# Performance work log

Measured on AMD Instinct MI355X. Metric: run time of the kernel, lower is better.

The kernel has to match this reference:

```python
import jax, jax.numpy as jnp
import numpy as np

NUM_SITES = 64
PHYS_DIM = 2
BOND_DIM = 32
BATCH = 65536


def _build_mps(num_sites, phys_dim, bond_dim, seed=0):
    """Replicates ImprovedMPS._initialize_tensors + _canonical_form, then
    zero-pads ragged cores into a dense [S, D, p, D] stack."""
    rng = np.random.default_rng(seed)
    tensors = []
    cur = 1
    for i in range(num_sites):
        if i == 0:
            nb = min(bond_dim, phys_dim)
            shape = (1, phys_dim, nb)
            cur = nb
        elif i == num_sites - 1:
            shape = (cur, phys_dim, 1)
        else:
            nb = min(bond_dim, cur * phys_dim)
            shape = (cur, phys_dim, nb)
            cur = nb
        ld, rd = shape[0] * shape[1], shape[2]
        m = (rng.standard_normal((ld, rd)) * 0.1).astype(np.float32)
        if ld >= rd:
            q, _ = np.linalg.qr(m)
            t = q.reshape(shape)
        else:
            q, _ = np.linalg.qr(m.T)
            t = q.T.reshape(shape)
        tensors.append(t.astype(np.float32))
    # left-canonical sweep
    for i in range(num_sites - 1):
        l, p, r = tensors[i].shape
        q, rr = np.linalg.qr(tensors[i].reshape(l * p, r))
        tensors[i] = q.reshape(l, p, q.shape[1]).astype(np.float32)
        nl, npd, nr = tensors[i + 1].shape
        tensors[i + 1] = (rr @ tensors[i + 1].reshape(nl, npd * nr)).reshape(rr.shape[0], npd, nr).astype(np.float32)
    # zero-pad ragged bonds into dense stack [S, D, p, D]
    A = np.zeros((num_sites, bond_dim, phys_dim, bond_dim), dtype=np.float32)
    for i, t in enumerate(tensors):
        l, p, r = t.shape
        A[i, :l, :, :r] = t
    return A


def setup_inputs() -> dict:
    key = jax.random.key(0)
    x_batch = jax.random.normal(key, (BATCH, NUM_SITES, PHYS_DIM), dtype=jnp.float32)
    A = jnp.asarray(_build_mps(NUM_SITES, PHYS_DIM, BOND_DIM))
    return {"x_batch": x_batch, "A": A}


def reference(x_batch, A):
    # x_batch: [B, S, p]; A: [S, D, p, D] (zero-padded ragged MPS cores)
    B = x_batch.shape[0]
    D = A.shape[1]
    # left_vector starts as ones(B,1) in the ragged view == one-hot e0 in padded view
    left0 = jnp.zeros((B, D), dtype=x_batch.dtype).at[:, 0].set(1.0)
    xs = jnp.moveaxis(x_batch, 1, 0)  # [S, B, p]

    def step(left, inp):
        A_i, x_i = inp  # [D, p, D], [B, p]
        # fuses: contracted = einsum('bp,lpd->bld'); left = einsum('bl,bld->bd')
        left = jnp.einsum('bl,bp,lpd->bd', left, x_i, A_i)
        return left, None

    left, _ = jax.lax.scan(step, left0, (A, xs))
    return left[:, :1]  # last core has right bond 1 -> only col 0 is nonzero
```

## Files before the change

### kernel.cpp

```cpp
#include <hip/hip_runtime.h>


typedef _Float16 half8 __attribute__((ext_vector_type(8)));
typedef _Float16 half4 __attribute__((ext_vector_type(4)));
typedef float floatx16 __attribute__((ext_vector_type(16)));
typedef float f32x4 __attribute__((ext_vector_type(4)));

#define NPAIRS 32
#define GCH 8192
#define XSTRIDE 129

__global__ void mps_prep_pair(const float* __restrict__ A, _Float16* __restrict__ Gf) {
    __shared__ float sA0[2048], sA1[2048], sG[4096];
    const int P = blockIdx.x, tid = threadIdx.x;
    const float* a0p = A + (size_t)(2 * P) * 2048;
    const float* a1p = A + (size_t)(2 * P + 1) * 2048;
#pragma unroll
    for (int i = 0; i < 8; ++i) {
        sA0[tid + 256 * i] = a0p[tid + 256 * i];
        sA1[tid + 256 * i] = a1p[tid + 256 * i];
    }
    __syncthreads();
    {
        const int l = tid >> 3, pq = (tid >> 1) & 3, dh16 = (tid & 1) * 16;
        const int p = pq >> 1, q = pq & 1;
        float accv[16];
#pragma unroll
        for (int dd = 0; dd < 16; ++dd) accv[dd] = 0.f;
        for (int m = 0; m < 32; ++m) {
            const float av = sA0[l * 64 + p * 32 + m];
            const float* bp = &sA1[m * 64 + q * 32 + dh16];
#pragma unroll
            for (int dd = 0; dd < 16; ++dd) accv[dd] += av * bp[dd];
        }
#pragma unroll
        for (int dd = 0; dd < 16; ++dd) sG[l * 128 + pq * 32 + dh16 + dd] = accv[dd];
    }
    __syncthreads();
    const int lane = tid & 63;
    const int h    = lane >> 5;
    const int d    = lane & 31;
#pragma unroll
    for (int pass = 0; pass < 2; ++pass) {
        const int kf = (tid >> 6) + pass * 4;
        const int pq = kf >> 1, lh = kf & 1;
        half8 v;
#pragma unroll
        for (int e = 0; e < 8; ++e) {
            const int l = 16 * lh + (e & 3) + 8 * (e >> 2) + 4 * h;
            v[e] = (_Float16)sG[l * 128 + pq * 32 + d];
        }
        reinterpret_cast<half8*>(Gf)[((size_t)P * 8 + kf) * 64 + lane] = v;
    }
}

#define MF32(A_, B_, C_) __builtin_amdgcn_mfma_f32_32x32x16_f16(A_, B_, C_, 0, 0, 0)

#define STAGEG(C, BUF)                                                        \
    {                                                                         \
        _Pragma("unroll")                                                     \
        for (int r_ = 0; r_ < 4; ++r_) {                                      \
            const int rec_ = r_ * 4 + wid;                                    \
            const _Float16* g_ = Gf + (size_t)(C) * GCH + rec_ * 512 + lane * 8; \
            __builtin_amdgcn_global_load_lds(                                 \
                (const __attribute__((address_space(1))) void*)g_,            \
                (__attribute__((address_space(3))) void*)&smG[(BUF) * GCH + rec_ * 512], \
                16, 0, 0);                                                    \
        }                                                                     \
    }

#define PAIRDO(BUF, LP, P)                                                    \
    {                                                                         \
        const half4 xq_ = smX[(P) * XSTRIDE + r];                             \
        const _Float16 w00_ = xq_[0] * xq_[2];                                \
        const _Float16 w01_ = xq_[0] * xq_[3];                                \
        const _Float16 w10_ = xq_[1] * xq_[2];                                \
        const _Float16 w11_ = xq_[1] * xq_[3];                                \
        half8 G_[8];                                                          \
        _Pragma("unroll")                                                     \
        for (int f_ = 0; f_ < 8; ++f_)                                        \
            G_[f_] = *(const half8*)&smG[(BUF) * GCH + (((LP) * 8 + f_) * 64 + lane) * 8]; \
        half8 FA0_, FA1_;                                                     \
        _Pragma("unroll")                                                     \
        for (int i_ = 0; i_ < 8; ++i_) {                                      \
            FA0_[i_] = (_Float16)acc[i_];                                     \
            FA1_[i_] = (_Float16)acc[8 + i_];                                 \
        }                                                                     \
        floatx16 t_;                                                          \
        t_ = MF32(G_[0], FA0_ * w00_, zv);                                    \
        t_ = MF32(G_[1], FA1_ * w00_, t_);                                    \
        t_ = MF32(G_[2], FA0_ * w01_, t_);                                    \
        t_ = MF32(G_[3], FA1_ * w01_, t_);                                    \
        t_ = MF32(G_[4], FA0_ * w10_, t_);                                    \
        t_ = MF32(G_[5], FA1_ * w10_, t_);                                    \
        t_ = MF32(G_[6], FA0_ * w11_, t_);                                    \
        t_ = MF32(G_[7], FA1_ * w11_, t_);                                    \
        acc = t_;                                                             \
    }

#define CHUNK(C, BUF)                                                         \
    {                                                                         \
        if ((C) < 15) STAGEG((C) + 1, 1 - (BUF));                             \
        PAIRDO(BUF, 0, 2 * (C))                                               \
        PAIRDO(BUF, 1, 2 * (C) + 1)                                           \
        __syncthreads();                                                      \
    }

__global__ __launch_bounds__(256, 2) void mps_main(const float* __restrict__ x,
                                                   const _Float16* __restrict__ Gf,
                                                   float* __restrict__ out) {
    __shared__ __align__(16) _Float16 smG[2 * GCH];
    __shared__ __align__(8)  half4    smX[32 * XSTRIDE];

    const int tid  = threadIdx.x;
    const int lane = tid & 63;
    const int wid  = tid >> 6;
    const int brow = blockIdx.x * 128;
    const int col  = lane & 31;
    const int r    = wid * 32 + col;

    STAGEG(0, 0);

#pragma unroll
    for (int i = 0; i < 16; ++i) {
        const int j   = i * 256 + tid;
        const int row = j >> 5, q = j & 31;
        const f32x4 v = *(const f32x4*)(x + (size_t)(brow + row) * 128 + 4 * q);
        half4 hv;
        hv[0] = (_Float16)v[0]; hv[1] = (_Float16)v[1];
        hv[2] = (_Float16)v[2]; hv[3] = (_Float16)v[3];
        smX[q * XSTRIDE + row] = hv;
    }

    floatx16 zv;
#pragma unroll
    for (int i = 0; i < 16; ++i) zv[i] = 0.f;

    floatx16 acc;
#pragma unroll
    for (int i = 0; i < 16; ++i) acc[i] = 0.f;
    if (lane < 32) acc[0] = 1.f;

    __syncthreads();

    CHUNK(0, 0)   CHUNK(1, 1)   CHUNK(2, 0)   CHUNK(3, 1)
    CHUNK(4, 0)   CHUNK(5, 1)   CHUNK(6, 0)   CHUNK(7, 1)
    CHUNK(8, 0)   CHUNK(9, 1)   CHUNK(10, 0)  CHUNK(11, 1)
    CHUNK(12, 0)  CHUNK(13, 1)  CHUNK(14, 0)  CHUNK(15, 1)

    if (lane < 32) out[brow + wid * 32 + lane] = acc[0];
}

extern "C" void kernel_launch(void* const* d_in, const int* in_sizes, int n_in,
                              void* d_out, int out_size, void* d_ws, size_t ws_size,
                              hipStream_t stream) {
    const float* x = (const float*)d_in[0];
    const float* A = (const float*)d_in[1];
    float* outp = (float*)d_out;
    _Float16* Gf = (_Float16*)d_ws;

    hipLaunchKernelGGL(mps_prep_pair, dim3(NPAIRS), dim3(256), 0, stream, A, Gf);
    hipLaunchKernelGGL(mps_main, dim3(65536 / 128), dim3(256), 0, stream, x, Gf, outp);
}
```

Baseline: 28.77 us.

## Split pair-core staging between LDS and direct register prefetch from global

The main kernel now stages only half of each fused pair-core (the p=0 fragments) into LDS. The other half comes straight from global memory into registers, prefetched one pair ahead with ping-pong register arrays. Because each LDS chunk now covers four pairs instead of two, the number of barriers and LDS traffic are halved. The cost is more VGPR pressure and per-lane global loads on the MFMA critical path. The prep kernel also moves to 512 threads, each doing half the output columns.

```diff
diff --git a/kernel.cpp b/kernel.cpp
--- a/kernel.cpp
+++ b/kernel.cpp
@@ -7,7 +7,7 @@
 typedef float f32x4 __attribute__((ext_vector_type(4)));
 
 #define NPAIRS 32
-#define GCH 8192
+#define GCHH 8192
 #define XSTRIDE 129
 
 __global__ void mps_prep_pair(const float* __restrict__ A, _Float16* __restrict__ Gf) {
@@ -16,42 +16,41 @@
     const float* a0p = A + (size_t)(2 * P) * 2048;
     const float* a1p = A + (size_t)(2 * P + 1) * 2048;
 #pragma unroll
-    for (int i = 0; i < 8; ++i) {
-        sA0[tid + 256 * i] = a0p[tid + 256 * i];
-        sA1[tid + 256 * i] = a1p[tid + 256 * i];
+    for (int i = 0; i < 4; ++i) {
+        sA0[tid + 512 * i] = a0p[tid + 512 * i];
+        sA1[tid + 512 * i] = a1p[tid + 512 * i];
     }
     __syncthreads();
     {
-        const int l = tid >> 3, pq = (tid >> 1) & 3, dh16 = (tid & 1) * 16;
+        const int item = tid >> 1;
+        const int l = item >> 3, pq = (item >> 1) & 3, dh16 = (item & 1) * 16;
+        const int ddb = (tid & 1) * 8;
         const int p = pq >> 1, q = pq & 1;
-        float accv[16];
+        float accv[8];
 #pragma unroll
-        for (int dd = 0; dd < 16; ++dd) accv[dd] = 0.f;
+        for (int dd = 0; dd < 8; ++dd) accv[dd] = 0.f;
         for (int m = 0; m < 32; ++m) {
             const float av = sA0[l * 64 + p * 32 + m];
-            const float* bp = &sA1[m * 64 + q * 32 + dh16];
+            const float* bp = &sA1[m * 64 + q * 32 + dh16 + ddb];
 #pragma unroll
-            for (int dd = 0; dd < 16; ++dd) accv[dd] += av * bp[dd];
+            for (int dd = 0; dd < 8; ++dd) accv[dd] += av * bp[dd];
         }
 #pragma unroll
-        for (int dd = 0; dd < 16; ++dd) sG[l * 128 + pq * 32 + dh16 + dd] = accv[dd];
+        for (int dd = 0; dd < 8; ++dd) sG[l * 128 + pq * 32 + dh16 + ddb + dd] = accv[dd];
     }
     __syncthreads();
     const int lane = tid & 63;
     const int h    = lane >> 5;
     const int d    = lane & 31;
+    const int kf   = tid >> 6;
+    const int pq   = kf >> 1, lh = kf & 1;
+    half8 v;
 #pragma unroll
-    for (int pass = 0; pass < 2; ++pass) {
-        const int kf = (tid >> 6) + pass * 4;
-        const int pq = kf >> 1, lh = kf & 1;
-        half8 v;
-#pragma unroll
-        for (int e = 0; e < 8; ++e) {
-            const int l = 16 * lh + (e & 3) + 8 * (e >> 2) + 4 * h;
-            v[e] = (_Float16)sG[l * 128 + pq * 32 + d];
-        }
-        reinterpret_cast<half8*>(Gf)[((size_t)P * 8 + kf) * 64 + lane] = v;
+    for (int e = 0; e < 8; ++e) {
+        const int l = 16 * lh + (e & 3) + 8 * (e >> 2) + 4 * h;
+        v[e] = (_Float16)sG[l * 128 + pq * 32 + d];
     }
+    reinterpret_cast<half8*>(Gf)[((size_t)P * 8 + kf) * 64 + lane] = v;
 }
 
 #define MF32(A_, B_, C_) __builtin_amdgcn_mfma_f32_32x32x16_f16(A_, B_, C_, 0, 0, 0)
@@ -61,25 +60,29 @@
         _Pragma("unroll")                                                     \
         for (int r_ = 0; r_ < 4; ++r_) {                                      \
             const int rec_ = r_ * 4 + wid;                                    \
-            const _Float16* g_ = Gf + (size_t)(C) * GCH + rec_ * 512 + lane * 8; \
+            const int pl_ = rec_ >> 2, kf_ = rec_ & 3;                        \
+            const _Float16* g_ = Gf + ((((size_t)(C) * 4 + pl_) * 8 + kf_) * 64 + lane) * 8; \
             __builtin_amdgcn_global_load_lds(                                 \
                 (const __attribute__((address_space(1))) void*)g_,            \
-                (__attribute__((address_space(3))) void*)&smG[(BUF) * GCH + rec_ * 512], \
+                (__attribute__((address_space(3))) void*)&smG[(BUF) * GCHH + rec_ * 512], \
                 16, 0, 0);                                                    \
         }                                                                     \
     }
 
-#define PAIRDO(BUF, LP, P)                                                    \
+#define PAIRDO(BUF, LP, P, GP, GN)                                            \
     {                                                                         \
         const half4 xq_ = smX[(P) * XSTRIDE + r];                             \
         const _Float16 w00_ = xq_[0] * xq_[2];                                \
         const _Float16 w01_ = xq_[0] * xq_[3];                                \
         const _Float16 w10_ = xq_[1] * xq_[2];                                \
         const _Float16 w11_ = xq_[1] * xq_[3];                                \
-        half8 G_[8];                                                          \
+        half8 GL_[4];                                                         \
         _Pragma("unroll")                                                     \
-        for (int f_ = 0; f_ < 8; ++f_)                                        \
-            G_[f_] = *(const half8*)&smG[(BUF) * GCH + (((LP) * 8 + f_) * 64 + lane) * 8]; \
+        for (int f_ = 0; f_ < 4; ++f_)                                        \
+            GL_[f_] = *(const half8*)&smG[(BUF) * GCHH + (((LP) * 4 + f_) * 64 + lane) * 8]; \
+        _Pragma("unroll")                                                     \
+        for (int f_ = 0; f_ < 4; ++f_)                                        \
+            GN[f_] = gfp[((((P) + 1) & 31) * 8 + 4 + f_) * 64 + lane];        \
         half8 FA0_, FA1_;                                                     \
         _Pragma("unroll")                                                     \
         for (int i_ = 0; i_ < 8; ++i_) {                                      \
@@ -87,29 +90,31 @@
             FA1_[i_] = (_Float16)acc[8 + i_];                                 \
         }                                                                     \
         floatx16 t_;                                                          \
-        t_ = MF32(G_[0], FA0_ * w00_, zv);                                    \
-        t_ = MF32(G_[1], FA1_ * w00_, t_);                                    \
-        t_ = MF32(G_[2], FA0_ * w01_, t_);                                    \
-        t_ = MF32(G_[3], FA1_ * w01_, t_);                                    \
-        t_ = MF32(G_[4], FA0_ * w10_, t_);                                    \
-        t_ = MF32(G_[5], FA1_ * w10_, t_);                                    \
-        t_ = MF32(G_[6], FA0_ * w11_, t_);                                    \
-        t_ = MF32(G_[7], FA1_ * w11_, t_);                                    \
+        t_ = MF32(GL_[0], FA0_ * w00_, zv);                                   \
+        t_ = MF32(GL_[1], FA1_ * w00_, t_);                                   \
+        t_ = MF32(GL_[2], FA0_ * w01_, t_);                                   \
+        t_ = MF32(GL_[3], FA1_ * w01_, t_);                                   \
+        t_ = MF32(GP[0], FA0_ * w10_, t_);                                    \
+        t_ = MF32(GP[1], FA1_ * w10_, t_);                                    \
+        t_ = MF32(GP[2], FA0_ * w11_, t_);                                    \
+        t_ = MF32(GP[3], FA1_ * w11_, t_);                                    \
         acc = t_;                                                             \
     }
 
 #define CHUNK(C, BUF)                                                         \
     {                                                                         \
-        if ((C) < 15) STAGEG((C) + 1, 1 - (BUF));                             \
-        PAIRDO(BUF, 0, 2 * (C))                                               \
-        PAIRDO(BUF, 1, 2 * (C) + 1)                                           \
+        if ((C) < 7) STAGEG((C) + 1, 1 - (BUF));                              \
+        PAIRDO(BUF, 0, 4 * (C) + 0, Ga, Gb)                                   \
+        PAIRDO(BUF, 1, 4 * (C) + 1, Gb, Ga)                                   \
+        PAIRDO(BUF, 2, 4 * (C) + 2, Ga, Gb)                                   \
+        PAIRDO(BUF, 3, 4 * (C) + 3, Gb, Ga)                                   \
         __syncthreads();                                                      \
     }
 
 __global__ __launch_bounds__(256, 2) void mps_main(const float* __restrict__ x,
                                                    const _Float16* __restrict__ Gf,
                                                    float* __restrict__ out) {
-    __shared__ __align__(16) _Float16 smG[2 * GCH];
+    __shared__ __align__(16) _Float16 smG[2 * GCHH];
     __shared__ __align__(8)  half4    smX[32 * XSTRIDE];
 
     const int tid  = threadIdx.x;
@@ -118,6 +123,8 @@
     const int brow = blockIdx.x * 128;
     const int col  = lane & 31;
     const int r    = wid * 32 + col;
+
+    const half8* gfp = reinterpret_cast<const half8*>(Gf);
 
     STAGEG(0, 0);
 
@@ -141,12 +148,14 @@
     for (int i = 0; i < 16; ++i) acc[i] = 0.f;
     if (lane < 32) acc[0] = 1.f;
 
+    half8 Ga[4], Gb[4];
+#pragma unroll
+    for (int f = 0; f < 4; ++f) Ga[f] = gfp[(0 * 8 + 4 + f) * 64 + lane];
+
     __syncthreads();
 
-    CHUNK(0, 0)   CHUNK(1, 1)   CHUNK(2, 0)   CHUNK(3, 1)
-    CHUNK(4, 0)   CHUNK(5, 1)   CHUNK(6, 0)   CHUNK(7, 1)
-    CHUNK(8, 0)   CHUNK(9, 1)   CHUNK(10, 0)  CHUNK(11, 1)
-    CHUNK(12, 0)  CHUNK(13, 1)  CHUNK(14, 0)  CHUNK(15, 1)
+    CHUNK(0, 0)  CHUNK(1, 1)  CHUNK(2, 0)  CHUNK(3, 1)
+    CHUNK(4, 0)  CHUNK(5, 1)  CHUNK(6, 0)  CHUNK(7, 1)
 
     if (lane < 32) out[brow + wid * 32 + lane] = acc[0];
 }
@@ -159,6 +168,6 @@
     float* outp = (float*)d_out;
     _Float16* Gf = (_Float16*)d_ws;
 
-    hipLaunchKernelGGL(mps_prep_pair, dim3(NPAIRS), dim3(256), 0, stream, A, Gf);
+    hipLaunchKernelGGL(mps_prep_pair, dim3(NPAIRS), dim3(512), 0, stream, A, Gf);
     hipLaunchKernelGGL(mps_main, dim3(65536 / 128), dim3(256), 0, stream, x, Gf, outp);
 }
```

After: 30.21 us. 5.0% more time.
